# Kernel tuning notes

Hardware: AMD Instinct MI355X
Metric: run time of the kernel (lower is better)

Reference implementation:

```python
import jax, jax.numpy as jnp
import numpy as np
from jax import lax


def _pairwise_dist(a, b):
    # a: (T, D), b: (T, D) -> (T, T) Euclidean distances via GEMM trick
    a2 = jnp.sum(a * a, axis=-1)
    b2 = jnp.sum(b * b, axis=-1)
    sq = a2[:, None] + b2[None, :] - 2.0 * (a @ b.T)
    return jnp.sqrt(jnp.maximum(sq, 1e-12))


def _frechet(seq1, seq2):
    cost = _pairwise_dist(seq1, seq2)  # (T, T)
    ca0 = lax.cummax(cost[0])          # first row boundary: running max

    def row_step(prev, cost_row):
        # prev: ca[i-1, :]; cost_row: cost[i, :]
        c0 = jnp.maximum(prev[0], cost_row[0])  # first-column boundary

        def col_step(left, x):
            c, up, diag = x
            val = jnp.maximum(c, jnp.minimum(jnp.minimum(up, left), diag))
            return val, val

        _, rest = lax.scan(col_step, c0, (cost_row[1:], prev[1:], prev[:-1]))
        cur = jnp.concatenate([c0[None], rest])
        return cur, None

    final_row, _ = lax.scan(row_step, ca0, cost[1:])
    return final_row[-1]


def setup_inputs() -> dict:
    key = jax.random.key(0)
    k1, k2 = jax.random.split(key)
    B, T, D = 32, 1024, 64
    pred = jax.random.normal(k1, (B, T, D), dtype=jnp.float32)
    targ = jax.random.normal(k2, (B, T, D), dtype=jnp.float32)
    return {"pred": pred, "targ": targ}


def reference(pred, targ):
    dists = jax.vmap(_frechet)(pred, targ)  # (B,)
    return jnp.mean(dists)
```

## Files before the change

kernel.cpp:

```cpp
#include <hip/hip_runtime.h>
#include <hip/hip_fp16.h>
#include <math.h>

#define T_LEN 1024
#define D_DIM 64
#define BATCH 32

#define SKEW_ROWS 1104
#define SKEW_STRIDE ((size_t)SKEW_ROWS * T_LEN)
#define PD 8

typedef __attribute__((ext_vector_type(2))) _Float16 h2v;

static __device__ __forceinline__ _Float16 hmin_(_Float16 a, _Float16 b) {
#if __has_builtin(__builtin_fminf16)
    return __builtin_fminf16(a, b);
#else
    return (b < a) ? b : a;
#endif
}
static __device__ __forceinline__ _Float16 hmax_(_Float16 a, _Float16 b) {
#if __has_builtin(__builtin_fmaxf16)
    return __builtin_fmaxf16(a, b);
#else
    return (a < b) ? b : a;
#endif
}
static __device__ __forceinline__ _Float16 med3h_(_Float16 a, _Float16 b, _Float16 c) {
#if __has_builtin(__builtin_amdgcn_fmed3h)
    return __builtin_amdgcn_fmed3h(a, b, c);
#else
    return hmax_(a, hmin_(b, c));
#endif
}

__global__ __launch_bounds__(128) void fill_stairs_kernel(__half* __restrict__ ws) {
    int s = blockIdx.x;
    int b = blockIdx.y;
    int tid = threadIdx.x;
    int col0 = 16 * (s + 1);
    int n_u4 = (T_LEN - col0) >> 3;
    if (tid < n_u4) {
        __half* row = ws + (size_t)b * SKEW_STRIDE + (size_t)s * T_LEN + col0;
        ((uint4*)row)[tid] = make_uint4(0x7C007C00u, 0x7C007C00u, 0x7C007C00u, 0x7C007C00u);
    }
}

__global__ __launch_bounds__(256) void cost_kernel(const float* __restrict__ pred,
                                                   const float* __restrict__ targ,
                                                   __half* __restrict__ skew_base) {
    const int b = blockIdx.z;
    const float* P = pred + (size_t)b * T_LEN * D_DIM;
    const float* T = targ + (size_t)b * T_LEN * D_DIM;
    __half* C = skew_base + (size_t)b * SKEW_STRIDE;
    const int row0 = blockIdx.y * 128;
    const int col0 = blockIdx.x * 128;

    __shared__ __align__(16) float ps[32][132];
    __shared__ __align__(16) float ts[32][132];
    __shared__ float p2[128], t2[128];

    const int tid = threadIdx.x;

    {
        int r = tid & 127;
        const float* src = (tid < 128) ? (P + (size_t)(row0 + r) * D_DIM)
                                       : (T + (size_t)(col0 + r) * D_DIM);
        float s = 0.0f;
#pragma unroll
        for (int q = 0; q < 16; q++) {
            float4 v = ((const float4*)src)[q];
            s += v.x * v.x + v.y * v.y + v.z * v.z + v.w * v.w;
        }
        if (tid < 128) p2[r] = s; else t2[r] = s;
    }

    const int lane = tid & 63, wv = tid >> 6;
    const int TX = (lane & 7) + 8 * (wv & 1);
    const int TY = (lane >> 3) + 8 * (wv >> 1);

    float acc[8][8];
#pragma unroll
    for (int i = 0; i < 8; i++)
#pragma unroll
        for (int j = 0; j < 8; j++) acc[i][j] = 0.0f;

#pragma unroll
    for (int chunk = 0; chunk < 2; ++chunk) {
        __syncthreads();
#pragma unroll
        for (int it = 0; it < 4; ++it) {
            int idx = tid + 256 * it;
            int row = idx >> 3;
            int kc = idx & 7;
            float4 v = *(const float4*)(P + (size_t)(row0 + row) * D_DIM + 32 * chunk + 4 * kc);
            ps[4 * kc + 0][row] = v.x; ps[4 * kc + 1][row] = v.y;
            ps[4 * kc + 2][row] = v.z; ps[4 * kc + 3][row] = v.w;
            float4 w = *(const float4*)(T + (size_t)(col0 + row) * D_DIM + 32 * chunk + 4 * kc);
            ts[4 * kc + 0][row] = w.x; ts[4 * kc + 1][row] = w.y;
            ts[4 * kc + 2][row] = w.z; ts[4 * kc + 3][row] = w.w;
        }
        __syncthreads();

#pragma unroll
        for (int kk = 0; kk < 32; ++kk) {
            float4 a0 = *(const float4*)&ps[kk][8 * TY];
            float4 a1 = *(const float4*)&ps[kk][8 * TY + 4];
            float4 b0 = *(const float4*)&ts[kk][8 * TX];
            float4 b1 = *(const float4*)&ts[kk][8 * TX + 4];
            float av[8] = {a0.x, a0.y, a0.z, a0.w, a1.x, a1.y, a1.z, a1.w};
            float bv[8] = {b0.x, b0.y, b0.z, b0.w, b1.x, b1.y, b1.z, b1.w};
#pragma unroll
            for (int i = 0; i < 8; i++)
#pragma unroll
                for (int j = 0; j < 8; j++) acc[i][j] += av[i] * bv[j];
        }
    }
    __syncthreads();

    const int skew = (col0 >> 4) + (TX >> 1);
#pragma unroll
    for (int i = 0; i < 8; i++) {
        float pa = p2[8 * TY + i];
        h2v o2[4];
#pragma unroll
        for (int j = 0; j < 4; j++) {
            float d0 = pa + t2[8 * TX + 2 * j]     - 2.0f * acc[i][2 * j];
            float d1 = pa + t2[8 * TX + 2 * j + 1] - 2.0f * acc[i][2 * j + 1];
            h2v h;
            h[0] = (_Float16)sqrtf(fmaxf(d0, 1e-12f));
            h[1] = (_Float16)sqrtf(fmaxf(d1, 1e-12f));
            o2[j] = h;
        }
        float4 st;
        st.x = __builtin_bit_cast(float, o2[0]);
        st.y = __builtin_bit_cast(float, o2[1]);
        st.z = __builtin_bit_cast(float, o2[2]);
        st.w = __builtin_bit_cast(float, o2[3]);
        __half* dst = C + (size_t)(row0 + 8 * TY + i + skew) * T_LEN + col0 + 8 * TX;
        *(float4*)dst = st;
    }
}


#define CELL(c_, pv_) { \
    _Float16 c = (c_); \
    _Float16 e = hmin_(pv_, diag); \
    _Float16 hm = hmax_(e, c); \
    _Float16 vv = med3h_(c, hm, left); \
    diag = pv_; pv_ = vv; left = vv; }

#define DP_STEP(PA, PB) { \
    int inc = __shfl_up(ro_bits, 1, 64); \
    _Float16 inch = __builtin_bit_cast(_Float16, (unsigned short)inc); \
    _Float16 left = (t == 0) ? lane0_left : inch; \
    _Float16 diag = (t == 0) ? HINF : diag_feed; \
    diag_feed = inch; \
    h2v u0 = __builtin_bit_cast(h2v, PA.x), u1 = __builtin_bit_cast(h2v, PA.y); \
    h2v u2 = __builtin_bit_cast(h2v, PA.z), u3 = __builtin_bit_cast(h2v, PA.w); \
    h2v u4 = __builtin_bit_cast(h2v, PB.x), u5 = __builtin_bit_cast(h2v, PB.y); \
    h2v u6 = __builtin_bit_cast(h2v, PB.z), u7 = __builtin_bit_cast(h2v, PB.w); \
    CELL(u0[0], v0)  CELL(u0[1], v1)  CELL(u1[0], v2)  CELL(u1[1], v3) \
    CELL(u2[0], v4)  CELL(u2[1], v5)  CELL(u3[0], v6)  CELL(u3[1], v7) \
    CELL(u4[0], v8)  CELL(u4[1], v9)  CELL(u5[0], v10) CELL(u5[1], v11) \
    CELL(u6[0], v12) CELL(u6[1], v13) CELL(u7[0], v14) CELL(u7[1], v15) \
    ro_bits = (int)(unsigned)__builtin_bit_cast(unsigned short, left); \
    lane0_left = HINF; }

#define RELOAD(n) { \
    __builtin_amdgcn_sched_barrier(0); \
    { const float4* p4 = (const float4*)q##n; \
      a##n = p4[0]; b##n = p4[1]; \
      q##n += (size_t)PD * T_LEN; } \
    __builtin_amdgcn_sched_barrier(0); }

#define INIT_SLOT(n) { \
    const float4* p4 = (const float4*)(Lp + (size_t)n * T_LEN); \
    a##n = p4[0]; b##n = p4[1]; \
    q##n = Lp + (size_t)(n + PD) * T_LEN; }

__global__ __launch_bounds__(64, 1) void dp_kernel_nb(const __half* __restrict__ cost,
                                                      float* __restrict__ out) {
    const int b = blockIdx.x;
    const int t = threadIdx.x;
    const _Float16 HINF = __builtin_bit_cast(_Float16, (unsigned short)0x7C00);
    const __half* Lp = cost + (size_t)b * SKEW_STRIDE + 16 * t;

    _Float16 v0 = HINF, v1 = HINF, v2 = HINF, v3 = HINF, v4 = HINF, v5 = HINF, v6 = HINF, v7 = HINF;
    _Float16 v8 = HINF, v9 = HINF, v10 = HINF, v11 = HINF, v12 = HINF, v13 = HINF, v14 = HINF, v15 = HINF;
    _Float16 diag_feed = HINF;
    _Float16 lane0_left = __builtin_bit_cast(_Float16, (unsigned short)0xFC00);
    int ro_bits = 0x7C00;

    float4 a0, b0, a1, b1, a2, b2, a3, b3, a4, b4, a5, b5, a6, b6, a7, b7;
    const __half *q0, *q1, *q2, *q3, *q4, *q5, *q6, *q7;
    INIT_SLOT(0) INIT_SLOT(1) INIT_SLOT(2) INIT_SLOT(3)
    INIT_SLOT(4) INIT_SLOT(5) INIT_SLOT(6) INIT_SLOT(7)

#pragma unroll 1
    for (int chunk = 0; chunk < 135; ++chunk) {
        DP_STEP(a0, b0) RELOAD(0)
        DP_STEP(a1, b1) RELOAD(1)
        DP_STEP(a2, b2) RELOAD(2)
        DP_STEP(a3, b3) RELOAD(3)
        DP_STEP(a4, b4) RELOAD(4)
        DP_STEP(a5, b5) RELOAD(5)
        DP_STEP(a6, b6) RELOAD(6)
        DP_STEP(a7, b7) RELOAD(7)
    }
    DP_STEP(a0, b0)
    DP_STEP(a1, b1)
    DP_STEP(a2, b2)
    DP_STEP(a3, b3)
    DP_STEP(a4, b4)
    DP_STEP(a5, b5)
    DP_STEP(a6, b6)

    if (t == 63) atomicAdd(out, (float)v15 * (1.0f / (float)BATCH));
}

__global__ __launch_bounds__(64) void dp_fused_kernel(const float* __restrict__ pred,
                                                      const float* __restrict__ targ,
                                                      float* __restrict__ out) {
    const int b = blockIdx.x;
    const int t = threadIdx.x;
    const float INF = __builtin_inff();
    const float* P = pred + (size_t)b * T_LEN * D_DIM;
    const float* T = targ + (size_t)b * T_LEN * D_DIM + (size_t)(16 * t) * D_DIM;

    float prev[16];
#pragma unroll
    for (int j = 0; j < 16; j++) prev[j] = INF;
    float right_out = INF;
    float diag_feed = INF;

    for (int s = 0; s < T_LEN + 63; s++) {
        int r = s - t;
        float inc = __shfl_up(right_out, 1, 64);
        float left = inc, diag = diag_feed;
        diag_feed = inc;
        if (t == 0) { left = (r == 0) ? -INF : INF; diag = INF; }
        if (r >= 0 && r < T_LEN) {
            float4 pr[16];
            const float4* pp = (const float4*)(P + (size_t)r * D_DIM);
#pragma unroll
            for (int q = 0; q < 16; q++) pr[q] = pp[q];
#pragma unroll
            for (int j = 0; j < 16; j++) {
                const float4* tp = (const float4*)(T + (size_t)j * D_DIM);
                float acc = 0.0f;
#pragma unroll
                for (int q = 0; q < 16; q++) {
                    float4 tv = tp[q];
                    float dx = pr[q].x - tv.x; acc += dx * dx;
                    float dy = pr[q].y - tv.y; acc += dy * dy;
                    float dz = pr[q].z - tv.z; acc += dz * dz;
                    float dw = pr[q].w - tv.w; acc += dw * dw;
                }
                float c = sqrtf(fmaxf(acc, 1e-12f));
                float e = fminf(prev[j], diag);
                float hm = fmaxf(e, c);
                float vv = fmaxf(c, fminf(hm, left));
                diag = prev[j];
                prev[j] = vv;
                left = vv;
            }
            right_out = left;
        }
    }
    if (t == 63) atomicAdd(out, prev[15] * (1.0f / (float)BATCH));
}

extern "C" void kernel_launch(void* const* d_in, const int* in_sizes, int n_in,
                              void* d_out, int out_size, void* d_ws, size_t ws_size,
                              hipStream_t stream) {
    const float* pred = (const float*)d_in[0];
    const float* targ = (const float*)d_in[1];
    float* out = (float*)d_out;

    hipMemsetAsync(out, 0, sizeof(float) * out_size, stream);

    const size_t need = (size_t)BATCH * SKEW_STRIDE * sizeof(__half);

    if (ws_size >= need) {
        __half* ws = (__half*)d_ws;
        fill_stairs_kernel<<<dim3(63, 32), 128, 0, stream>>>(ws);
        cost_kernel<<<dim3(8, 8, BATCH), 256, 0, stream>>>(pred, targ, ws);
        dp_kernel_nb<<<BATCH, 64, 0, stream>>>(ws, out);
    } else {
        dp_fused_kernel<<<BATCH, 64, 0, stream>>>(pred, targ, out);
    }
}
```

Measured before the change: 381.5 us.

## Add producer wave streaming cost rows into LDS ring for DP consumer

Replaces the single-wave DP kernel, which loaded skewed cost rows from global memory into registers eight steps ahead, with a two-wave block. A producer wave copies rows into a 32-slot LDS ring using global_load_lds, and the consumer wave runs the DP reading from LDS with a one-step register prefetch. The two waves hand off through workgroup-scope atomic counters and sleep-polling. The aim is to hide global load latency on the serial wavefront chain, at the cost of spin-wait synchronisation overhead and LDS read latency on the critical path.

```diff
diff --git a/kernel.cpp b/kernel.cpp
--- a/kernel.cpp
+++ b/kernel.cpp
@@ -8,7 +8,9 @@
 
 #define SKEW_ROWS 1104
 #define SKEW_STRIDE ((size_t)SKEW_ROWS * T_LEN)
-#define PD 8
+
+#define RING_SLOTS 32
+#define NBATCH 136
 
 typedef __attribute__((ext_vector_type(2))) _Float16 h2v;
 
@@ -142,6 +144,13 @@
     }
 }
 
+
+__device__ __forceinline__ void gll16(const __half* g, __half* l) {
+    __builtin_amdgcn_global_load_lds(
+        (const __attribute__((address_space(1))) void*)g,
+        (__attribute__((address_space(3))) void*)l,
+        16, 0, 0);
+}
 
 #define CELL(c_, pv_) { \
     _Float16 c = (c_); \
@@ -167,56 +176,87 @@
     ro_bits = (int)(unsigned)__builtin_bit_cast(unsigned short, left); \
     lane0_left = HINF; }
 
-#define RELOAD(n) { \
-    __builtin_amdgcn_sched_barrier(0); \
-    { const float4* p4 = (const float4*)q##n; \
-      a##n = p4[0]; b##n = p4[1]; \
-      q##n += (size_t)PD * T_LEN; } \
-    __builtin_amdgcn_sched_barrier(0); }
-
-#define INIT_SLOT(n) { \
-    const float4* p4 = (const float4*)(Lp + (size_t)n * T_LEN); \
-    a##n = p4[0]; b##n = p4[1]; \
-    q##n = Lp + (size_t)(n + PD) * T_LEN; }
-
-__global__ __launch_bounds__(64, 1) void dp_kernel_nb(const __half* __restrict__ cost,
-                                                      float* __restrict__ out) {
+#define CSTEP(u, kk, PFGUARD) { \
+    float4 cur0 = nxt0, cur1 = nxt1; \
+    if ((u) < (PFGUARD)) { \
+        const float4* np = (const float4*)(lb + (size_t)((8 * (kk) + (u) + 1) & 31) * 2048); \
+        nxt0 = np[0]; nxt1 = np[1]; \
+    } \
+    DP_STEP(cur0, cur1) }
+
+__global__ __launch_bounds__(128, 1) void dp_kernel_pc(const __half* __restrict__ cost,
+                                                       float* __restrict__ out) {
+    __shared__ __align__(16) __half ring[RING_SLOTS][T_LEN];
+    __shared__ int prod_done;
+    __shared__ int cons_done;
+
     const int b = blockIdx.x;
-    const int t = threadIdx.x;
-    const _Float16 HINF = __builtin_bit_cast(_Float16, (unsigned short)0x7C00);
-    const __half* Lp = cost + (size_t)b * SKEW_STRIDE + 16 * t;
-
-    _Float16 v0 = HINF, v1 = HINF, v2 = HINF, v3 = HINF, v4 = HINF, v5 = HINF, v6 = HINF, v7 = HINF;
-    _Float16 v8 = HINF, v9 = HINF, v10 = HINF, v11 = HINF, v12 = HINF, v13 = HINF, v14 = HINF, v15 = HINF;
-    _Float16 diag_feed = HINF;
-    _Float16 lane0_left = __builtin_bit_cast(_Float16, (unsigned short)0xFC00);
-    int ro_bits = 0x7C00;
-
-    float4 a0, b0, a1, b1, a2, b2, a3, b3, a4, b4, a5, b5, a6, b6, a7, b7;
-    const __half *q0, *q1, *q2, *q3, *q4, *q5, *q6, *q7;
-    INIT_SLOT(0) INIT_SLOT(1) INIT_SLOT(2) INIT_SLOT(3)
-    INIT_SLOT(4) INIT_SLOT(5) INIT_SLOT(6) INIT_SLOT(7)
-
-#pragma unroll 1
-    for (int chunk = 0; chunk < 135; ++chunk) {
-        DP_STEP(a0, b0) RELOAD(0)
-        DP_STEP(a1, b1) RELOAD(1)
-        DP_STEP(a2, b2) RELOAD(2)
-        DP_STEP(a3, b3) RELOAD(3)
-        DP_STEP(a4, b4) RELOAD(4)
-        DP_STEP(a5, b5) RELOAD(5)
-        DP_STEP(a6, b6) RELOAD(6)
-        DP_STEP(a7, b7) RELOAD(7)
-    }
-    DP_STEP(a0, b0)
-    DP_STEP(a1, b1)
-    DP_STEP(a2, b2)
-    DP_STEP(a3, b3)
-    DP_STEP(a4, b4)
-    DP_STEP(a5, b5)
-    DP_STEP(a6, b6)
-
-    if (t == 63) atomicAdd(out, (float)v15 * (1.0f / (float)BATCH));
+    const int wave = threadIdx.x >> 6;
+    const int t = threadIdx.x & 63;
+    const __half* gbase = cost + (size_t)b * SKEW_STRIDE;
+
+    if (threadIdx.x == 0) { prod_done = 0; cons_done = 0; }
+    __syncthreads();
+
+    if (wave == 1) {
+        for (int k = 0; k < NBATCH; ++k) {
+            while (__hip_atomic_load(&cons_done, __ATOMIC_ACQUIRE,
+                                     __HIP_MEMORY_SCOPE_WORKGROUP) < k - 3) {
+                __builtin_amdgcn_s_sleep(1);
+            }
+            const __half* gr = gbase + (size_t)(8 * k) * T_LEN;
+#pragma unroll
+            for (int u = 0; u < 8; ++u) {
+                int slot = (8 * k + u) & 31;
+                const __half* g = gr + (size_t)u * T_LEN;
+                gll16(g + 8 * t, &ring[slot][0]);
+                gll16(g + 512 + 8 * t, &ring[slot][512]);
+            }
+            __builtin_amdgcn_s_waitcnt(0);
+            if (t == 0) {
+                __hip_atomic_store(&prod_done, k + 1, __ATOMIC_RELEASE,
+                                   __HIP_MEMORY_SCOPE_WORKGROUP);
+            }
+        }
+    } else {
+        const _Float16 HINF = __builtin_bit_cast(_Float16, (unsigned short)0x7C00);
+        _Float16 v0 = HINF, v1 = HINF, v2 = HINF, v3 = HINF, v4 = HINF, v5 = HINF, v6 = HINF, v7 = HINF;
+        _Float16 v8 = HINF, v9 = HINF, v10 = HINF, v11 = HINF, v12 = HINF, v13 = HINF, v14 = HINF, v15 = HINF;
+        _Float16 diag_feed = HINF;
+        _Float16 lane0_left = __builtin_bit_cast(_Float16, (unsigned short)0xFC00);
+        int ro_bits = 0x7C00;
+
+        const char* lb = (const char*)&ring[0][0] + 32 * t;
+        float4 nxt0, nxt1;
+
+        for (int k = 0; k < 135; ++k) {
+            while (__hip_atomic_load(&prod_done, __ATOMIC_ACQUIRE,
+                                     __HIP_MEMORY_SCOPE_WORKGROUP) < k + 1) {
+                __builtin_amdgcn_s_sleep(1);
+            }
+            {
+                const float4* np = (const float4*)(lb + (size_t)((8 * k) & 31) * 2048);
+                nxt0 = np[0]; nxt1 = np[1];
+            }
+            CSTEP(0, k, 7) CSTEP(1, k, 7) CSTEP(2, k, 7) CSTEP(3, k, 7)
+            CSTEP(4, k, 7) CSTEP(5, k, 7) CSTEP(6, k, 7) CSTEP(7, k, 7)
+            __hip_atomic_store(&cons_done, k + 1, __ATOMIC_RELEASE,
+                               __HIP_MEMORY_SCOPE_WORKGROUP);
+        }
+        while (__hip_atomic_load(&prod_done, __ATOMIC_ACQUIRE,
+                                 __HIP_MEMORY_SCOPE_WORKGROUP) < 136) {
+            __builtin_amdgcn_s_sleep(1);
+        }
+        {
+            const float4* np = (const float4*)(lb + (size_t)((8 * 135) & 31) * 2048);
+            nxt0 = np[0]; nxt1 = np[1];
+        }
+        CSTEP(0, 135, 6) CSTEP(1, 135, 6) CSTEP(2, 135, 6)
+        CSTEP(3, 135, 6) CSTEP(4, 135, 6) CSTEP(5, 135, 6)
+        CSTEP(6, 135, 6)
+
+        if (t == 63) atomicAdd(out, (float)v15 * (1.0f / (float)BATCH));
+    }
 }
 
 __global__ __launch_bounds__(64) void dp_fused_kernel(const float* __restrict__ pred,
@@ -286,7 +326,7 @@
         __half* ws = (__half*)d_ws;
         fill_stairs_kernel<<<dim3(63, 32), 128, 0, stream>>>(ws);
         cost_kernel<<<dim3(8, 8, BATCH), 256, 0, stream>>>(pred, targ, ws);
-        dp_kernel_nb<<<BATCH, 64, 0, stream>>>(ws, out);
+        dp_kernel_pc<<<BATCH, 128, 0, stream>>>(ws, out);
     } else {
         dp_fused_kernel<<<BATCH, 64, 0, stream>>>(pred, targ, out);
     }
```

Result: faster. 366.8 us (-3.9%).
